# Performance work log

Hardware: AMD Instinct MI355X
Metric: run time of the kernel (lower is better)

The kernel has to match this reference:

```python
import jax, jax.numpy as jnp
from jax import lax
import numpy as np

EPS = 1e-5  # torch BatchNorm1d default eps
N_OUT = 8   # action dim -> 8x8 NAF matrix


def _bn_train(x, g, b):
    # torch BatchNorm1d in train mode: biased batch stats over the batch axis
    m = x.mean(0)
    v = ((x - m) ** 2).mean(0)
    return g * (x - m) / jnp.sqrt(v + EPS) + b


def _branch(seg, wc, bc, wo, bo):
    # seg: [2,8] -> view [1,2,8]; conv1d(2->16,k4,p1) -> [1,16,7]; relu; maxpool2 -> [1,16,3]
    x = seg.reshape(1, 2, 8)
    y = lax.conv_general_dilated(x, wc, window_strides=(1,), padding=[(1, 1)],
                                 dimension_numbers=('NCH', 'OIH', 'NCH')) + bc[None, :, None]
    y = jax.nn.relu(y)
    y = y[..., :6].reshape(1, 16, 3, 2).max(-1)  # non-overlapping maxpool, drops last elem
    y = y.reshape(1, 48) @ wo.T + bo             # Linear(48,16)
    return y.reshape(2, 8)


def setup_inputs() -> dict:
    key = jax.random.key(0)
    ks = iter(jax.random.split(key, 32))
    r = lambda shape, s=1.0: s * jax.random.normal(next(ks), shape, dtype=jnp.float32)
    inp = {
        'inputs': r((2, 32)),
        'u': r((2, 8)),
        'w1c': r((16, 2, 4), 0.2), 'b1c': r((16,), 0.1), 'w1o': r((16, 48), 0.1), 'b1o': r((16,), 0.1),
        'w2c': r((16, 2, 4), 0.2), 'b2c': r((16,), 0.1), 'w2o': r((16, 48), 0.1), 'b2o': r((16,), 0.1),
        'w3c': r((16, 2, 4), 0.2), 'b3c': r((16,), 0.1), 'w3o': r((16, 48), 0.1), 'b3o': r((16,), 0.1),
        'g0': jnp.ones((32,), jnp.float32), 'be0': jnp.zeros((32,), jnp.float32),
        'W1': r((128, 32), 0.1), 'bl1': r((128,), 0.1),
        'W2': r((128, 128), 0.1), 'bl2': r((128,), 0.1),
        'Vw': r((1, 128), 0.1), 'Vb': r((1,), 0.1),
        'Mw': r((8, 128), 0.1), 'Mb': r((8,), 0.1),
        'Lw': r((64, 128), 0.1), 'Lb': r((64,), 0.1),
    }
    return inp


def reference(inputs, u, w1c, b1c, w1o, b1o, w2c, b2c, w2o, b2o, w3c, b3c, w3o, b3o,
              g0, be0, W1, bl1, W2, bl2, Vw, Vb, Mw, Mb, Lw, Lb):
    c1 = _branch(inputs[:, 0:8], w1c, b1c, w1o, b1o)
    c2 = _branch(inputs[:, 8:16], w2c, b2c, w2o, b2o)
    c3 = _branch(inputs[:, 16:24], w3c, b3c, w3o, b3o)
    x = jnp.concatenate([c1, c2, c3, inputs[:, 24:]], axis=1)  # [2, num_inputs]
    x = _bn_train(x, g0, be0)
    x = jnp.tanh(x @ W1.T + bl1)
    x = jnp.tanh(x @ W2.T + bl2)
    V = x @ Vw.T + Vb                        # [2,1]
    mu = jnp.tanh(x @ Mw.T + Mb)             # [2,8]
    L = (x @ Lw.T + Lb).reshape(-1, N_OUT, N_OUT)
    tril = jnp.tril(jnp.ones((N_OUT, N_OUT), jnp.float32), -1)
    diag = jnp.eye(N_OUT, dtype=jnp.float32)
    L = L * tril + jnp.exp(L) * diag         # strict lower + exp diagonal
    P = jnp.einsum('bij,bkj->bik', L, L)     # L @ L^T
    d = u - mu
    A = -0.5 * jnp.einsum('bi,bij,bj->b', d, P, d)[:, None]
    Q = A + V
    return (mu, Q, V)
```

## Files before the change

kernel.cpp:

```cpp
#include <hip/hip_runtime.h>

#define BN_EPS 1e-5f

__global__ __launch_bounds__(256) void naf_policy_kernel(
    const float* __restrict__ inputs, const float* __restrict__ u,
    const float* __restrict__ w1c, const float* __restrict__ b1c,
    const float* __restrict__ w1o, const float* __restrict__ b1o,
    const float* __restrict__ w2c, const float* __restrict__ b2c,
    const float* __restrict__ w2o, const float* __restrict__ b2o,
    const float* __restrict__ w3c, const float* __restrict__ b3c,
    const float* __restrict__ w3o, const float* __restrict__ b3o,
    const float* __restrict__ g0, const float* __restrict__ be0,
    const float* __restrict__ W1, const float* __restrict__ bl1,
    const float* __restrict__ W2, const float* __restrict__ bl2,
    const float* __restrict__ Vw, const float* __restrict__ Vb,
    const float* __restrict__ Mw, const float* __restrict__ Mb,
    const float* __restrict__ Lw, const float* __restrict__ Lb,
    float* __restrict__ out)
{
    __shared__ float pooled[3][48];
    __shared__ float xcat[2][32];
    __shared__ float xn[2][32];
    __shared__ float h1[2][128];
    __shared__ float h2[2][128];
    __shared__ float Lm[2][8][8];
    __shared__ float mu_s[2][8];
    __shared__ float V_s[2];

    const int tid = threadIdx.x;

    if (tid < 144) {
        const int br = tid / 48;
        const int n  = tid % 48;
        const int o  = n / 3;
        const int p  = n % 3;
        const float* wc = (br == 0) ? w1c : (br == 1 ? w2c : w3c);
        const float* bc = (br == 0) ? b1c : (br == 1 ? b2c : b3c);
        const float* seg = inputs + br * 8;
        float best = 0.0f;
        #pragma unroll
        for (int dt = 0; dt < 2; ++dt) {
            const int t = 2 * p + dt;
            float acc = bc[o];
            #pragma unroll
            for (int c = 0; c < 2; ++c) {
                #pragma unroll
                for (int k = 0; k < 4; ++k) {
                    const int pos = t + k - 1;
                    const float xv = (pos >= 0 && pos < 8) ? seg[c * 32 + pos] : 0.0f;
                    acc = fmaf(xv, wc[o * 8 + c * 4 + k], acc);
                }
            }
            acc = fmaxf(acc, 0.0f);
            best = fmaxf(best, acc);
        }
        pooled[br][n] = best;
    } else if (tid < 160) {
        const int q = tid - 144;
        const int r = q >> 3, col = q & 7;
        xcat[r][24 + col] = inputs[r * 32 + 24 + col];
    }
    __syncthreads();

    if (tid < 48) {
        const int br = tid / 16;
        const int j  = tid % 16;
        const float* wo = (br == 0) ? w1o : (br == 1 ? w2o : w3o);
        const float* bo = (br == 0) ? b1o : (br == 1 ? b2o : b3o);
        float acc = bo[j];
        #pragma unroll 8
        for (int n = 0; n < 48; ++n)
            acc = fmaf(pooled[br][n], wo[j * 48 + n], acc);
        const int r = j >> 3, col = j & 7;
        xcat[r][br * 8 + col] = acc;
    }
    __syncthreads();

    if (tid < 32) {
        const float a = xcat[0][tid], b = xcat[1][tid];
        const float m = 0.5f * (a + b);
        const float da = a - m, db = b - m;
        const float v = 0.5f * (da * da + db * db);
        const float inv = rsqrtf(v + BN_EPS);
        const float g = g0[tid], be = be0[tid];
        xn[0][tid] = fmaf(g * da, inv, be);
        xn[1][tid] = fmaf(g * db, inv, be);
    }
    __syncthreads();

    {
        const int r = tid >> 7, j = tid & 127;
        float acc = bl1[j];
        const float* w = W1 + j * 32;
        #pragma unroll 8
        for (int k = 0; k < 32; ++k) acc = fmaf(xn[r][k], w[k], acc);
        h1[r][j] = tanhf(acc);
    }
    __syncthreads();

    {
        const int r = tid >> 7, j = tid & 127;
        float acc = bl2[j];
        const float* w = W2 + j * 128;
        #pragma unroll 8
        for (int k = 0; k < 128; ++k) acc = fmaf(h1[r][k], w[k], acc);
        h2[r][j] = tanhf(acc);
    }
    __syncthreads();

    if (tid < 128) {
        const int r = tid >> 6, idx = tid & 63;
        float acc = Lb[idx];
        const float* w = Lw + idx * 128;
        #pragma unroll 8
        for (int k = 0; k < 128; ++k) acc = fmaf(h2[r][k], w[k], acc);
        const int i = idx >> 3, jj = idx & 7;
        float val;
        if (jj < i)       val = acc;
        else if (jj == i) val = expf(acc);
        else              val = 0.0f;
        Lm[r][i][jj] = val;
    } else if (tid < 144) {
        const int q = tid - 128;
        const int r = q >> 3, j = q & 7;
        float acc = Mb[j];
        const float* w = Mw + j * 128;
        #pragma unroll 8
        for (int k = 0; k < 128; ++k) acc = fmaf(h2[r][k], w[k], acc);
        const float m = tanhf(acc);
        mu_s[r][j] = m;
        out[r * 8 + j] = m;
    } else if (tid < 146) {
        const int r = tid - 144;
        float acc = Vb[0];
        #pragma unroll 8
        for (int k = 0; k < 128; ++k) acc = fmaf(h2[r][k], Vw[k], acc);
        V_s[r] = acc;
        out[18 + r] = acc;
    }
    __syncthreads();

    if (tid < 2) {
        const int r = tid;
        float d[8];
        #pragma unroll
        for (int j = 0; j < 8; ++j) d[j] = u[r * 8 + j] - mu_s[r][j];
        float s = 0.0f;
        #pragma unroll
        for (int k = 0; k < 8; ++k) {
            float c = 0.0f;
            #pragma unroll
            for (int i = 0; i < 8; ++i) c = fmaf(d[i], Lm[r][i][k], c);
            s = fmaf(c, c, s);
        }
        out[16 + r] = fmaf(-0.5f, s, V_s[r]);
    }
}

extern "C" void kernel_launch(void* const* d_in, const int* in_sizes, int n_in,
                              void* d_out, int out_size, void* d_ws, size_t ws_size,
                              hipStream_t stream) {
    (void)in_sizes; (void)n_in; (void)d_ws; (void)ws_size; (void)out_size;
    const float* inputs = (const float*)d_in[0];
    const float* u      = (const float*)d_in[1];
    const float* w1c    = (const float*)d_in[2];
    const float* b1c    = (const float*)d_in[3];
    const float* w1o    = (const float*)d_in[4];
    const float* b1o    = (const float*)d_in[5];
    const float* w2c    = (const float*)d_in[6];
    const float* b2c    = (const float*)d_in[7];
    const float* w2o    = (const float*)d_in[8];
    const float* b2o    = (const float*)d_in[9];
    const float* w3c    = (const float*)d_in[10];
    const float* b3c    = (const float*)d_in[11];
    const float* w3o    = (const float*)d_in[12];
    const float* b3o    = (const float*)d_in[13];
    const float* g0     = (const float*)d_in[14];
    const float* be0    = (const float*)d_in[15];
    const float* W1     = (const float*)d_in[16];
    const float* bl1    = (const float*)d_in[17];
    const float* W2     = (const float*)d_in[18];
    const float* bl2    = (const float*)d_in[19];
    const float* Vw     = (const float*)d_in[20];
    const float* Vb     = (const float*)d_in[21];
    const float* Mw     = (const float*)d_in[22];
    const float* Mb     = (const float*)d_in[23];
    const float* Lw     = (const float*)d_in[24];
    const float* Lb     = (const float*)d_in[25];

    naf_policy_kernel<<<1, 256, 0, stream>>>(
        inputs, u, w1c, b1c, w1o, b1o, w2c, b2c, w2o, b2o, w3c, b3c, w3o, b3o,
        g0, be0, W1, bl1, W2, bl2, Vw, Vb, Mw, Mb, Lw, Lb, (float*)d_out);
}
```

Baseline: 115.2 us.

## Prefetch all MLP weights into LDS concurrently with conv stage

The block grows to 512 threads. 448 of them bulk-copy W1, W2, Lw, Mw and the biases into shared memory with float4 loads, while 64 threads compute the conv/pool branches. The dense layers then read weights from LDS, and each thread handles both batch rows with float4 dot products split across several accumulators. The goal is to overlap global weight-fetch latency with the early stages and to halve redundant weight reads. The cost is a large LDS footprint (about 120 KB) and fewer active threads in the later stages.

New measurement: 114.1 us. Within noise of the previous version (-1.0%).

```diff
diff --git a/kernel.cpp b/kernel.cpp
--- a/kernel.cpp
+++ b/kernel.cpp
@@ -2,7 +2,7 @@
 
 #define BN_EPS 1e-5f
 
-__global__ __launch_bounds__(256) void naf_policy_kernel(
+__global__ __launch_bounds__(512) void naf_policy_kernel(
     const float* __restrict__ inputs, const float* __restrict__ u,
     const float* __restrict__ w1c, const float* __restrict__ b1c,
     const float* __restrict__ w1o, const float* __restrict__ b1o,
@@ -18,47 +18,86 @@
     const float* __restrict__ Lw, const float* __restrict__ Lb,
     float* __restrict__ out)
 {
+    __shared__ alignas(16) float sW1[128 * 32];
+    __shared__ alignas(16) float sW2[128 * 128];
+    __shared__ alignas(16) float sLw[64 * 128];
+    __shared__ alignas(16) float sMw[8 * 128];
+    __shared__ alignas(16) float sVw[128];
+    __shared__ alignas(16) float sbl1[128];
+    __shared__ alignas(16) float sbl2[128];
+    __shared__ alignas(16) float sLb[64];
+    __shared__ alignas(16) float sMb[8];
+    __shared__ alignas(16) float su[16];
+    __shared__ float sVb;
     __shared__ float pooled[3][48];
     __shared__ float xcat[2][32];
-    __shared__ float xn[2][32];
-    __shared__ float h1[2][128];
-    __shared__ float h2[2][128];
+    __shared__ alignas(16) float xn[2][32];
+    __shared__ alignas(16) float h1[2][128];
+    __shared__ alignas(16) float h2[2][128];
     __shared__ float Lm[2][8][8];
     __shared__ float mu_s[2][8];
     __shared__ float V_s[2];
 
     const int tid = threadIdx.x;
 
-    if (tid < 144) {
-        const int br = tid / 48;
-        const int n  = tid % 48;
-        const int o  = n / 3;
-        const int p  = n % 3;
-        const float* wc = (br == 0) ? w1c : (br == 1 ? w2c : w3c);
-        const float* bc = (br == 0) ? b1c : (br == 1 ? b2c : b3c);
-        const float* seg = inputs + br * 8;
-        float best = 0.0f;
-        #pragma unroll
-        for (int dt = 0; dt < 2; ++dt) {
-            const int t = 2 * p + dt;
-            float acc = bc[o];
-            #pragma unroll
-            for (int c = 0; c < 2; ++c) {
+    if (tid >= 64) {
+        const int t = tid - 64;
+        {
+            const float4* s = (const float4*)W2; float4* d = (float4*)sW2;
+            #pragma unroll
+            for (int j = 0; j < 10; ++j) { int i = t + j * 448; if (i < 4096) d[i] = s[i]; }
+        }
+        {
+            const float4* s = (const float4*)Lw; float4* d = (float4*)sLw;
+            #pragma unroll
+            for (int j = 0; j < 5; ++j) { int i = t + j * 448; if (i < 2048) d[i] = s[i]; }
+        }
+        {
+            const float4* s = (const float4*)W1; float4* d = (float4*)sW1;
+            #pragma unroll
+            for (int j = 0; j < 3; ++j) { int i = t + j * 448; if (i < 1024) d[i] = s[i]; }
+        }
+        if (t < 256)                 ((float4*)sMw)[t]        = ((const float4*)Mw)[t];
+        else if (t < 288)            ((float4*)sVw)[t - 256]  = ((const float4*)Vw)[t - 256];
+        else if (t < 320)            ((float4*)sbl1)[t - 288] = ((const float4*)bl1)[t - 288];
+        else if (t < 352)            ((float4*)sbl2)[t - 320] = ((const float4*)bl2)[t - 320];
+        else if (t < 368)            ((float4*)sLb)[t - 352]  = ((const float4*)Lb)[t - 352];
+        else if (t < 370)            ((float4*)sMb)[t - 368]  = ((const float4*)Mb)[t - 368];
+        else if (t < 374)            ((float4*)su)[t - 370]   = ((const float4*)u)[t - 370];
+        else if (t == 374)           sVb = Vb[0];
+    } else {
+        for (int it = tid; it < 160; it += 64) {
+            if (it < 144) {
+                const int br = it / 48;
+                const int n  = it % 48;
+                const int o  = n / 3;
+                const int p  = n % 3;
+                const float* wc = (br == 0) ? w1c : (br == 1 ? w2c : w3c);
+                const float* bc = (br == 0) ? b1c : (br == 1 ? b2c : b3c);
+                const float* seg = inputs + br * 8;
+                float best = 0.0f;
                 #pragma unroll
-                for (int k = 0; k < 4; ++k) {
-                    const int pos = t + k - 1;
-                    const float xv = (pos >= 0 && pos < 8) ? seg[c * 32 + pos] : 0.0f;
-                    acc = fmaf(xv, wc[o * 8 + c * 4 + k], acc);
+                for (int dt = 0; dt < 2; ++dt) {
+                    const int tpos = 2 * p + dt;
+                    float acc = bc[o];
+                    #pragma unroll
+                    for (int c = 0; c < 2; ++c) {
+                        #pragma unroll
+                        for (int k = 0; k < 4; ++k) {
+                            const int pos = tpos + k - 1;
+                            const float xv = (pos >= 0 && pos < 8) ? seg[c * 32 + pos] : 0.0f;
+                            acc = fmaf(xv, wc[o * 8 + c * 4 + k], acc);
+                        }
+                    }
+                    best = fmaxf(best, fmaxf(acc, 0.0f));
                 }
+                pooled[br][n] = best;
+            } else {
+                const int q = it - 144;
+                const int r = q >> 3, col = q & 7;
+                xcat[r][24 + col] = inputs[r * 32 + 24 + col];
             }
-            acc = fmaxf(acc, 0.0f);
-            best = fmaxf(best, acc);
-        }
-        pooled[br][n] = best;
-    } else if (tid < 160) {
-        const int q = tid - 144;
-        const int r = q >> 3, col = q & 7;
-        xcat[r][24 + col] = inputs[r * 32 + 24 + col];
+        }
     }
     __syncthreads();
 
@@ -88,55 +127,101 @@
     }
     __syncthreads();
 
-    {
-        const int r = tid >> 7, j = tid & 127;
-        float acc = bl1[j];
-        const float* w = W1 + j * 32;
-        #pragma unroll 8
-        for (int k = 0; k < 32; ++k) acc = fmaf(xn[r][k], w[k], acc);
-        h1[r][j] = tanhf(acc);
-    }
-    __syncthreads();
-
-    {
-        const int r = tid >> 7, j = tid & 127;
-        float acc = bl2[j];
-        const float* w = W2 + j * 128;
-        #pragma unroll 8
-        for (int k = 0; k < 128; ++k) acc = fmaf(h1[r][k], w[k], acc);
-        h2[r][j] = tanhf(acc);
-    }
-    __syncthreads();
-
     if (tid < 128) {
-        const int r = tid >> 6, idx = tid & 63;
-        float acc = Lb[idx];
-        const float* w = Lw + idx * 128;
-        #pragma unroll 8
-        for (int k = 0; k < 128; ++k) acc = fmaf(h2[r][k], w[k], acc);
-        const int i = idx >> 3, jj = idx & 7;
-        float val;
-        if (jj < i)       val = acc;
-        else if (jj == i) val = expf(acc);
-        else              val = 0.0f;
-        Lm[r][i][jj] = val;
-    } else if (tid < 144) {
-        const int q = tid - 128;
-        const int r = q >> 3, j = q & 7;
-        float acc = Mb[j];
-        const float* w = Mw + j * 128;
-        #pragma unroll 8
-        for (int k = 0; k < 128; ++k) acc = fmaf(h2[r][k], w[k], acc);
-        const float m = tanhf(acc);
-        mu_s[r][j] = m;
-        out[r * 8 + j] = m;
-    } else if (tid < 146) {
-        const int r = tid - 144;
-        float acc = Vb[0];
-        #pragma unroll 8
-        for (int k = 0; k < 128; ++k) acc = fmaf(h2[r][k], Vw[k], acc);
-        V_s[r] = acc;
-        out[18 + r] = acc;
+        const float4* w  = (const float4*)(sW1 + tid * 32);
+        const float4* x0 = (const float4*)(&xn[0][0]);
+        const float4* x1 = (const float4*)(&xn[1][0]);
+        float s00 = 0.f, s01 = 0.f, s02 = 0.f, s03 = 0.f;
+        float s10 = 0.f, s11 = 0.f, s12 = 0.f, s13 = 0.f;
+        #pragma unroll
+        for (int k = 0; k < 8; ++k) {
+            const float4 wv = w[k], a = x0[k], b = x1[k];
+            s00 = fmaf(a.x, wv.x, s00); s01 = fmaf(a.y, wv.y, s01);
+            s02 = fmaf(a.z, wv.z, s02); s03 = fmaf(a.w, wv.w, s03);
+            s10 = fmaf(b.x, wv.x, s10); s11 = fmaf(b.y, wv.y, s11);
+            s12 = fmaf(b.z, wv.z, s12); s13 = fmaf(b.w, wv.w, s13);
+        }
+        const float bsum = sbl1[tid];
+        h1[0][tid] = tanhf(((s00 + s01) + (s02 + s03)) + bsum);
+        h1[1][tid] = tanhf(((s10 + s11) + (s12 + s13)) + bsum);
+    }
+    __syncthreads();
+
+    if (tid < 128) {
+        const float4* w  = (const float4*)(sW2 + tid * 128);
+        const float4* x0 = (const float4*)(&h1[0][0]);
+        const float4* x1 = (const float4*)(&h1[1][0]);
+        float s00 = 0.f, s01 = 0.f, s02 = 0.f, s03 = 0.f;
+        float s10 = 0.f, s11 = 0.f, s12 = 0.f, s13 = 0.f;
+        #pragma unroll 8
+        for (int k = 0; k < 32; ++k) {
+            const float4 wv = w[k], a = x0[k], b = x1[k];
+            s00 = fmaf(a.x, wv.x, s00); s01 = fmaf(a.y, wv.y, s01);
+            s02 = fmaf(a.z, wv.z, s02); s03 = fmaf(a.w, wv.w, s03);
+            s10 = fmaf(b.x, wv.x, s10); s11 = fmaf(b.y, wv.y, s11);
+            s12 = fmaf(b.z, wv.z, s12); s13 = fmaf(b.w, wv.w, s13);
+        }
+        const float bsum = sbl2[tid];
+        h2[0][tid] = tanhf(((s00 + s01) + (s02 + s03)) + bsum);
+        h2[1][tid] = tanhf(((s10 + s11) + (s12 + s13)) + bsum);
+    }
+    __syncthreads();
+
+    if (tid < 64) {
+        const float4* w  = (const float4*)(sLw + tid * 128);
+        const float4* x0 = (const float4*)(&h2[0][0]);
+        const float4* x1 = (const float4*)(&h2[1][0]);
+        float s00 = 0.f, s01 = 0.f, s02 = 0.f, s03 = 0.f;
+        float s10 = 0.f, s11 = 0.f, s12 = 0.f, s13 = 0.f;
+        #pragma unroll 8
+        for (int k = 0; k < 32; ++k) {
+            const float4 wv = w[k], a = x0[k], b = x1[k];
+            s00 = fmaf(a.x, wv.x, s00); s01 = fmaf(a.y, wv.y, s01);
+            s02 = fmaf(a.z, wv.z, s02); s03 = fmaf(a.w, wv.w, s03);
+            s10 = fmaf(b.x, wv.x, s10); s11 = fmaf(b.y, wv.y, s11);
+            s12 = fmaf(b.z, wv.z, s12); s13 = fmaf(b.w, wv.w, s13);
+        }
+        const float a0 = ((s00 + s01) + (s02 + s03)) + sLb[tid];
+        const float a1 = ((s10 + s11) + (s12 + s13)) + sLb[tid];
+        const int i = tid >> 3, jj = tid & 7;
+        float v0, v1;
+        if (jj < i)       { v0 = a0;       v1 = a1; }
+        else if (jj == i) { v0 = expf(a0); v1 = expf(a1); }
+        else              { v0 = 0.f;      v1 = 0.f; }
+        Lm[0][i][jj] = v0;
+        Lm[1][i][jj] = v1;
+    } else if (tid < 72) {
+        const int j = tid - 64;
+        const float4* w  = (const float4*)(sMw + j * 128);
+        const float4* x0 = (const float4*)(&h2[0][0]);
+        const float4* x1 = (const float4*)(&h2[1][0]);
+        float s0 = 0.f, s1 = 0.f;
+        #pragma unroll 8
+        for (int k = 0; k < 32; ++k) {
+            const float4 wv = w[k], a = x0[k], b = x1[k];
+            s0 = fmaf(a.x, wv.x, s0); s0 = fmaf(a.y, wv.y, s0);
+            s0 = fmaf(a.z, wv.z, s0); s0 = fmaf(a.w, wv.w, s0);
+            s1 = fmaf(b.x, wv.x, s1); s1 = fmaf(b.y, wv.y, s1);
+            s1 = fmaf(b.z, wv.z, s1); s1 = fmaf(b.w, wv.w, s1);
+        }
+        const float m0 = tanhf(s0 + sMb[j]);
+        const float m1 = tanhf(s1 + sMb[j]);
+        mu_s[0][j] = m0; mu_s[1][j] = m1;
+        out[j] = m0; out[8 + j] = m1;
+    } else if (tid < 74) {
+        const int r = tid - 72;
+        const float4* w = (const float4*)sVw;
+        const float4* x = (const float4*)(&h2[r][0]);
+        float s = 0.f;
+        #pragma unroll 8
+        for (int k = 0; k < 32; ++k) {
+            const float4 wv = w[k], a = x[k];
+            s = fmaf(a.x, wv.x, s); s = fmaf(a.y, wv.y, s);
+            s = fmaf(a.z, wv.z, s); s = fmaf(a.w, wv.w, s);
+        }
+        s += sVb;
+        V_s[r] = s;
+        out[18 + r] = s;
     }
     __syncthreads();
 
@@ -144,7 +229,7 @@
         const int r = tid;
         float d[8];
         #pragma unroll
-        for (int j = 0; j < 8; ++j) d[j] = u[r * 8 + j] - mu_s[r][j];
+        for (int j = 0; j < 8; ++j) d[j] = su[r * 8 + j] - mu_s[r][j];
         float s = 0.0f;
         #pragma unroll
         for (int k = 0; k < 8; ++k) {
@@ -188,7 +273,7 @@
     const float* Lw     = (const float*)d_in[24];
     const float* Lb     = (const float*)d_in[25];
 
-    naf_policy_kernel<<<1, 256, 0, stream>>>(
+    naf_policy_kernel<<<1, 512, 0, stream>>>(
         inputs, u, w1c, b1c, w1o, b1o, w2c, b2c, w2o, b2o, w3c, b3c, w3o, b3o,
         g0, be0, W1, bl1, W2, bl2, Vw, Vb, Mw, Mb, Lw, Lb, (float*)d_out);
 }
```
